# Kernel tuning notes

Hardware: AMD Instinct MI355X
Metric: run time of the kernel (lower is better)

## Reference

```python
import jax, jax.numpy as jnp
import numpy as np
from math import factorial

MAX_L = 2
B = 2
N = 256
TAU = 16


def _cg(j1, j2, j3, m1, m2, m3):
    # standard Clebsch-Gordan coefficient <j1 m1 j2 m2 | j3 m3> (Racah formula)
    if m1 + m2 != m3:
        return 0.0
    f = factorial
    pre = ((2 * j3 + 1) * f(j3 + j1 - j2) * f(j3 - j1 + j2) * f(j1 + j2 - j3) / f(j1 + j2 + j3 + 1)) ** 0.5
    pre *= (f(j3 + m3) * f(j3 - m3) * f(j1 - m1) * f(j1 + m1) * f(j2 - m2) * f(j2 + m2)) ** 0.5
    kmin = max(0, j2 - j3 - m1, j1 - j3 + m2)
    kmax = min(j1 + j2 - j3, j1 - m1, j2 + m2)
    s = 0.0
    for k in range(kmin, kmax + 1):
        s += (-1) ** k / (f(k) * f(j1 + j2 - j3 - k) * f(j1 - m1 - k) * f(j2 + m2 - k) * f(j3 - j2 + m1 + k) * f(j3 - j1 - m2 + k))
    return pre * s


def _cg_table(max_l):
    tab = {}
    for l1 in range(max_l + 1):
        for l2 in range(max_l + 1):
            for l in range(abs(l1 - l2), min(l1 + l2, max_l) + 1):
                C = np.zeros((2 * l1 + 1, 2 * l2 + 1, 2 * l + 1), dtype=np.float32)
                for m1 in range(-l1, l1 + 1):
                    for m2 in range(-l2, l2 + 1):
                        m = m1 + m2
                        if -l <= m <= l:
                            C[m1 + l1, m2 + l2, m + l] = _cg(l1, l2, l, m1, m2, m)
                tab[(l1, l2, l)] = jnp.asarray(C)
    return tab

CG_TAB = _cg_table(MAX_L)


def _cg_product(xs, ys, max_l):
    # xs[l]: [..., 2l+1, t1], ys[l]: [..., 2l+1, t2] -> out[l]: [..., 2l+1, sum t1*t2]
    outs = []
    for l in range(max_l + 1):
        blocks = []
        for l1 in range(max_l + 1):
            for l2 in range(max_l + 1):
                if abs(l1 - l2) <= l <= l1 + l2:
                    C = CG_TAB[(l1, l2, l)]
                    blk = jnp.einsum('...ic,...jd,ijk->...kcd', xs[l1], ys[l2], C)
                    blocks.append(blk.reshape(blk.shape[:-2] + (blk.shape[-2] * blk.shape[-1],)))
        outs.append(jnp.concatenate(blocks, axis=-1))
    return outs


TAU_CG_NL = [3 * TAU * TAU, 6 * TAU * TAU, 6 * TAU * TAU]  # (l1,l2) pair counts: 3,6,6
TAU_CG_REL = [3 * TAU, 6 * TAU, 6 * TAU]


def setup_inputs() -> dict:
    key = jax.random.key(0)
    ks = jax.random.split(key, 14)
    inp = {}
    for l in range(MAX_L + 1):
        inp['v%d' % l] = jax.random.normal(ks[l], (B, N, 1, 2 * l + 1, TAU), dtype=jnp.float32)
        inp['s%d' % l] = jax.random.normal(ks[3 + l], (B, N, N, 2 * l + 1, 1), dtype=jnp.float32)
        inp['wnl%d' % l] = jax.random.normal(ks[6 + l], (TAU_CG_NL[l], TAU), dtype=jnp.float32) * 0.05
        inp['wrel%d' % l] = jax.random.normal(ks[9 + l], (TAU_CG_REL[l], TAU), dtype=jnp.float32) * 0.05
    inp['conn'] = jax.random.randint(ks[13], (B, N, N), 0, 2, dtype=jnp.int32)
    return inp


def reference(v0, v1, v2, conn, s0, s1, s2, wnl0, wnl1, wnl2, wrel0, wrel1, wrel2):
    verts = [v0, v1, v2]
    sph = [s0, s1, s2]
    wnl = [wnl0, wnl1, wnl2]
    wrel = [wrel0, wrel1, wrel2]
    connf = conn.astype(v0.dtype)
    # masked message passing: aggregate neighbor features per node
    vmp = [jnp.einsum('bij,bjxmc->bixmc', connf, v) for v in verts]
    # node-level CG product with itself, then channel mixing
    cg_nl = _cg_product(vmp, vmp, MAX_L)
    mixed_nl = [p @ w for p, w in zip(cg_nl, wnl)]  # [B,N,1,2l+1,TAU]
    # repeat along second array dim to match sph adims [N,N]
    rep = [jnp.broadcast_to(p, (p.shape[0], p.shape[1], N) + p.shape[3:]) for p in mixed_nl]
    # edge-level CG product with spherical harmonics, then channel mixing
    cg_rel = _cg_product(rep, sph, MAX_L)
    mixed_rel = [p @ w for p, w in zip(cg_rel, wrel)]  # [B,N,N,2l+1,TAU]
    # sum over neighbor dim (axis 2), keepdim -> adims back to [N,1]
    summed = [jnp.sum(p, axis=2, keepdims=True) for p in mixed_rel]
    # NormalizeVecArr divides each part in-place by its total sum
    normed = [p / jnp.sum(p) for p in summed]
    return tuple(normed)
```

## Files before the change

kernel.cpp:

```cpp
#include <hip/hip_runtime.h>


#define TAU 16

#define PART_OFF 768
#define VMP_OFF  4096
#define S_OFF    77824
#define WT_OFF   86016

constexpr double cfact(int n){ double r=1.0; for(int i=2;i<=n;i++) r*=i; return r; }
constexpr double csqrt(double x){
  if (x<=0.0) return 0.0;
  double g = x<1.0 ? 1.0 : x;
  for (int i=0;i<80;i++) g = 0.5*(g + x/g);
  return g;
}
constexpr double cg_c(int j1,int j2,int j3,int m1,int m2,int m3){
  if (m1+m2 != m3) return 0.0;
  double pre = csqrt((2.0*j3+1.0)*cfact(j3+j1-j2)*cfact(j3-j1+j2)*cfact(j1+j2-j3)/cfact(j1+j2+j3+1));
  pre *= csqrt(cfact(j3+m3)*cfact(j3-m3)*cfact(j1-m1)*cfact(j1+m1)*cfact(j2-m2)*cfact(j2+m2));
  int kmin = 0;
  if (j2-j3-m1 > kmin) kmin = j2-j3-m1;
  if (j1-j3+m2 > kmin) kmin = j1-j3+m2;
  int kmax = j1+j2-j3;
  if (j1-m1 < kmax) kmax = j1-m1;
  if (j2+m2 < kmax) kmax = j2+m2;
  double s = 0.0;
  for (int k=kmin;k<=kmax;k++){
    double d = cfact(k)*cfact(j1+j2-j3-k)*cfact(j1-m1-k)*cfact(j2+m2-k)*cfact(j3-j2+m1+k)*cfact(j3-j1-m2+k);
    s += (k & 1) ? (-1.0/d) : (1.0/d);
  }
  return pre*s;
}
struct CGTab { float v[615]; };
constexpr CGTab gen_cg(){
  CGTab t{};
  const int TRI[15][3] = {
    {0,0,0},{0,1,1},{0,2,2},{1,0,1},{1,1,0},{1,1,1},{1,1,2},{1,2,1},{1,2,2},
    {2,0,2},{2,1,1},{2,1,2},{2,2,0},{2,2,1},{2,2,2}};
  int off = 0;
  for (int tr=0;tr<15;tr++){
    const int l1=TRI[tr][0], l2=TRI[tr][1], l=TRI[tr][2];
    for (int i1=0;i1<2*l1+1;i1++)
      for (int i2=0;i2<2*l2+1;i2++)
        for (int ik=0;ik<2*l+1;ik++)
          t.v[off++] = (float)cg_c(l1,l2,l,i1-l1,i2-l2,ik-l);
  }
  return t;
}
constexpr CGTab CG = gen_cg();

constexpr int OFF3[27] = {
  0,-1,-1,  -1,1,-1,   -1,-1,10,
  -1,35,-1, 44,53,80,  -1,125,170,
  -1,-1,245,-1,270,315,390,415,490};
constexpr int PAIRS[3][6][2] = {
  {{0,0},{1,1},{2,2},{0,0},{0,0},{0,0}},
  {{0,1},{1,0},{1,1},{1,2},{2,1},{2,2}},
  {{0,2},{1,1},{1,2},{2,0},{2,1},{2,2}}};
constexpr int VOFF[3]   = {0,16,64};
constexpr int SOFF[3]   = {0,1,4};
constexpr int OUT_OFF[3]= {0,8192,32768};
constexpr int NPAIR[3]  = {3,6,6};
constexpr int FOFF[9]   = {0,16,32,48,64,80,96,112,128};
constexpr int WROFF[3]  = {0,768,2304};
constexpr int WTL[3]    = {0,12288,36864};
constexpr int ROWB[3]   = {0,3,21};

__device__ constexpr int RIDX(int l, int mi){ return l==0 ? 0 : (l==1 ? 1+mi : 4+mi); }

__global__ __launch_bounds__(512)
void k_prep(const float* __restrict__ v0, const float* __restrict__ v1, const float* __restrict__ v2,
            const float* __restrict__ s0, const float* __restrict__ s1, const float* __restrict__ s2,
            const float* __restrict__ wnl0, const float* __restrict__ wnl1, const float* __restrict__ wnl2,
            const int* __restrict__ conn, float* __restrict__ ws)
{
  __shared__ float sh_conn[256];
  __shared__ float sh_v[2][144];
  const int t  = threadIdx.x;
  const int bi = blockIdx.x;
  const int b  = bi >> 8;

  if (t < 256) sh_conn[t] = (float)conn[((size_t)bi<<8) + t];
  __syncthreads();

  if (t < 288) {
    const int h = (t >= 144) ? 1 : 0;
    const int tt = t - h*144;
    int l, m, c;
    if (tt < 16)      { l=0; m=0;          c=tt;    }
    else if (tt < 64) { l=1; m=(tt-16)>>4; c=tt&15; }
    else              { l=2; m=(tt-64)>>4; c=tt&15; }
    const float* vl = (l==0) ? v0 : (l==1) ? v1 : v2;
    const int dm = 2*l+1;
    const int stride = dm*TAU;
    const float* base = vl + (((size_t)b*256 + h*128)*dm + m)*TAU + c;
    const float* cr = &sh_conn[h*128];
    float a[8];
    #pragma unroll
    for (int q=0;q<8;q++) a[q]=0.f;
    for (int j=0;j<128;j+=8){
      #pragma unroll
      for (int q=0;q<8;q++) a[q] += cr[j+q]*base[(j+q)*stride];
    }
    sh_v[h][tt] = ((a[0]+a[1])+(a[2]+a[3])) + ((a[4]+a[5])+(a[6]+a[7]));
  } else if (t >= 320 && t < 384) {
    const int lane = t - 320;
    const float* p0 = s0 + (size_t)bi*256;
    const float* p1 = s1 + (size_t)bi*768;
    const float* p2 = s2 + (size_t)bi*1280;
    float a[9];
    #pragma unroll
    for (int m=0;m<9;m++) a[m]=0.f;
    #pragma unroll
    for (int q=0;q<4;q++){
      const int j = lane + q*64;
      a[0] += p0[j];
      a[1] += p1[3*j+0]; a[2] += p1[3*j+1]; a[3] += p1[3*j+2];
      #pragma unroll
      for (int k=0;k<5;k++) a[4+k] += p2[5*j+k];
    }
    #pragma unroll
    for (int m=0;m<9;m++){
      #pragma unroll
      for (int off=32; off; off>>=1) a[m] += __shfl_xor(a[m], off);
    }
    if (lane == 0) {
      #pragma unroll
      for (int m=0;m<9;m++) ws[S_OFF + (size_t)bi*16 + m] = a[m];
    }
  } else if (t >= 448 && bi < 15) {
    const int tile = bi;
    const float* src = (tile<3) ? (wnl0 + (size_t)tile*4096)
                     : (tile<9) ? (wnl1 + (size_t)(tile-3)*4096)
                                : (wnl2 + (size_t)(tile-9)*4096);
    float* dst = ws + WT_OFF + (size_t)tile*4096;
    const int q = t - 448;
    #pragma unroll
    for (int r=0;r<4;r++){
      const int cd = q + r*64;
      const float4 r0 = *(const float4*)(src + cd*16);
      const float4 r1 = *(const float4*)(src + cd*16 + 4);
      const float4 r2 = *(const float4*)(src + cd*16 + 8);
      const float4 r3 = *(const float4*)(src + cd*16 + 12);
      dst[ 0*256+cd]=r0.x; dst[ 1*256+cd]=r0.y; dst[ 2*256+cd]=r0.z; dst[ 3*256+cd]=r0.w;
      dst[ 4*256+cd]=r1.x; dst[ 5*256+cd]=r1.y; dst[ 6*256+cd]=r1.z; dst[ 7*256+cd]=r1.w;
      dst[ 8*256+cd]=r2.x; dst[ 9*256+cd]=r2.y; dst[10*256+cd]=r2.z; dst[11*256+cd]=r2.w;
      dst[12*256+cd]=r3.x; dst[13*256+cd]=r3.y; dst[14*256+cd]=r3.z; dst[15*256+cd]=r3.w;
    }
  }
  __syncthreads();
  if (t < 144) ws[VMP_OFF + (size_t)bi*144 + t] = sh_v[0][t] + sh_v[1][t];
}

template<int L, int P>
__device__ __forceinline__ void build_p(float* __restrict__ dst,
                                        const float (&v_c)[9], const float (&v_d)[9], int tt){
  constexpr int l1 = PAIRS[L][P][0], l2 = PAIRS[L][P][1];
  constexpr int d2 = 2*l2+1, dkk = 2*L+1;
  constexpr int coff = OFF3[l1*9+l2*3+L];
  constexpr int row0 = ROWB[L] + P*dkk;
  #pragma unroll
  for (int kk=0; kk<dkk; kk++){
    const int m = kk - L;
    float a = 0.f;
    #pragma unroll
    for (int m1=-l1; m1<=l1; m1++){
      const int m2 = m - m1;
      if (m2 >= -l2 && m2 <= l2){
        const float C = CG.v[coff + ((m1+l1)*d2 + (m2+l2))*dkk + kk];
        a += C * v_c[RIDX(l1,m1+l1)] * v_d[RIDX(l2,m2+l2)];
      }
    }
    dst[(row0 + kk)*256 + tt] = a;
  }
}

template<int L>
__device__ __forceinline__ void mixl(const float* __restrict__ wt, const float* __restrict__ sh_bm,
                                     float* __restrict__ sh_mnl, int ksub, int tc0){
  constexpr int NP = NPAIR[L];
  constexpr int DK = 2*L+1;
  float acc[DK][2];
  #pragma unroll
  for (int k=0;k<DK;k++){ acc[k][0]=0.f; acc[k][1]=0.f; }
  const float* wb = wt + (size_t)tc0*256 + ksub*4;
  #pragma unroll
  for (int p=0;p<NP;p++){
    const float4 w0 = *(const float4*)(wb + (size_t)p*4096);
    const float4 w1 = *(const float4*)(wb + (size_t)p*4096 + 256);
    #pragma unroll
    for (int k=0;k<DK;k++){
      const float4 bk = *(const float4*)&sh_bm[(ROWB[L] + p*DK + k)*256 + ksub*4];
      acc[k][0] += bk.x*w0.x + bk.y*w0.y + bk.z*w0.z + bk.w*w0.w;
      acc[k][1] += bk.x*w1.x + bk.y*w1.y + bk.z*w1.z + bk.w*w1.w;
    }
  }
  #pragma unroll
  for (int k=0;k<DK;k++){
    #pragma unroll
    for (int off=32; off; off>>=1){
      acc[k][0] += __shfl_xor(acc[k][0], off);
      acc[k][1] += __shfl_xor(acc[k][1], off);
    }
  }
  if (ksub == 0) {
    #pragma unroll
    for (int k=0;k<DK;k++){
      sh_mnl[VOFF[L] + k*16 + tc0    ] = acc[k][0];
      sh_mnl[VOFF[L] + k*16 + tc0 + 1] = acc[k][1];
    }
  }
}

__global__ __launch_bounds__(512, 2)
void k_main(const float* __restrict__ wrel0, const float* __restrict__ wrel1, const float* __restrict__ wrel2,
            const float* __restrict__ ws, float* __restrict__ out, float* __restrict__ part)
{
  __shared__ __align__(16) float sh_bm[51*256];
  __shared__ float sh_wrel[3840];
  __shared__ float sh_mnl[144];
  __shared__ float sh_S[9];
  __shared__ float sh_rel[6*144];
  __shared__ float sh_acc[144];
  __shared__ float sh_lred[48];

  const int t  = threadIdx.x;
  const int bi = blockIdx.x;

  for (int i=t; i<3840; i+=512){
    float v;
    if (i < 768)       v = wrel0[i];
    else if (i < 2304) v = wrel1[i-768];
    else               v = wrel2[i-2304];
    sh_wrel[i] = v;
  }
  const int bc = (t>>4)&15, bd = t&15;
  float v_c[9], v_d[9];
  {
    const float* vb = ws + VMP_OFF + (size_t)bi*144;
    #pragma unroll
    for (int r=0;r<9;r++){ v_c[r] = vb[FOFF[r]+bc]; v_d[r] = vb[FOFF[r]+bd]; }
  }
  if (t < 9) sh_S[t] = ws[S_OFF + (size_t)bi*16 + t];

  const int tg = t>>6, ksub = t&63;
  const int tc0 = tg*2;

  {
    const int tt = t & 255;
    if (t < 256){
      build_p<0,0>(sh_bm,v_c,v_d,tt); build_p<0,1>(sh_bm,v_c,v_d,tt); build_p<0,2>(sh_bm,v_c,v_d,tt);
      build_p<1,0>(sh_bm,v_c,v_d,tt); build_p<1,1>(sh_bm,v_c,v_d,tt); build_p<1,2>(sh_bm,v_c,v_d,tt);
      build_p<2,0>(sh_bm,v_c,v_d,tt); build_p<2,1>(sh_bm,v_c,v_d,tt); build_p<2,2>(sh_bm,v_c,v_d,tt);
    } else {
      build_p<1,3>(sh_bm,v_c,v_d,tt); build_p<1,4>(sh_bm,v_c,v_d,tt); build_p<1,5>(sh_bm,v_c,v_d,tt);
      build_p<2,3>(sh_bm,v_c,v_d,tt); build_p<2,4>(sh_bm,v_c,v_d,tt); build_p<2,5>(sh_bm,v_c,v_d,tt);
    }
  }
  __syncthreads();
  mixl<0>(ws + WT_OFF + WTL[0], sh_bm, sh_mnl, ksub, tc0);
  mixl<1>(ws + WT_OFF + WTL[1], sh_bm, sh_mnl, ksub, tc0);
  mixl<2>(ws + WT_OFF + WTL[2], sh_bm, sh_mnl, ksub, tc0);
  __syncthreads();

  int l=0, f=0;
  if (t < 16)       { l=0; f=t;    }
  else if (t < 64)  { l=1; f=t-16; }
  else if (t < 144) { l=2; f=t-64; }
  const int k = f>>4, tc = f&15;

  if (t < 144) {
    const int np = NPAIR[l];
    #pragma unroll
    for (int p=0; p<6; p++) {
      if (p < np) {
        const int l1 = PAIRS[l][p][0], l2 = PAIRS[l][p][1];
        const int d2 = 2*l2+1;
        const int coff = OFF3[l1*9+l2*3+l];
        const int dk = 2*l+1;
        const int m = k - l;
        float a = 0.f;
        const int lo = (-l1 > m-l2) ? -l1 : m-l2;
        const int hi = ( l1 < m+l2) ?  l1 : m+l2;
        #pragma unroll
        for (int m1=-2; m1<=2; m1++) {
          if (m1 >= lo && m1 <= hi) {
            const int m2 = m - m1;
            const float C = CG.v[coff + ((m1+l1)*d2 + (m2+l2))*dk + k];
            a += C * sh_mnl[VOFF[l1] + (m1+l1)*TAU + tc] * sh_S[SOFF[l2] + (m2+l2)];
          }
        }
        sh_rel[p*144 + t] = a;
      }
    }
  }
  __syncthreads();
  if (t < 144) {
    const int np = NPAIR[l];
    float acc = 0.f;
    #pragma unroll
    for (int p=0; p<6; p++) {
      if (p < np) {
        const float* rrow = &sh_rel[p*144 + VOFF[l] + k*16];
        const float* wrow = &sh_wrel[WROFF[l] + p*256 + tc];
        #pragma unroll
        for (int c=0; c<16; c++)
          acc += rrow[c] * wrow[c*16];
      }
    }
    out[OUT_OFF[l] + ((size_t)bi*(2*l+1) + k)*TAU + tc] = acc;
    sh_acc[t] = acc;
  }
  __syncthreads();
  if (t < 48) {
    const int ll = t>>4, q = t&15;
    const int n = 2*ll+1;
    float a = 0.f;
    for (int i=0;i<n;i++) a += sh_acc[VOFF[ll] + i*16 + q];
    sh_lred[t] = a;
  }
  __syncthreads();
  if (t < 3) {
    float a = 0.f;
    #pragma unroll
    for (int q=0;q<16;q++) a += sh_lred[t*16+q];
    part[t*512 + bi] = a;
  }
}

__global__ __launch_bounds__(256)
void k_norm(float* __restrict__ out, const float* __restrict__ part){
  __shared__ float sh_r[96];
  __shared__ float sh_d[3];
  const int t = threadIdx.x;
  if (t < 96){
    const int l = t>>5, q = t&31;
    const float* p = part + l*512 + q*16;
    float a=0.f;
    #pragma unroll
    for (int i=0;i<16;i++) a += p[i];
    sh_r[t] = a;
  }
  __syncthreads();
  if (t < 3){
    float a=0.f;
    const float* r = &sh_r[t*32];
    #pragma unroll
    for (int i=0;i<32;i++) a += r[i];
    sh_d[t] = a;
  }
  __syncthreads();
  const int idx = blockIdx.x*256 + t;
  if (idx < 73728){
    const int l = (idx < 8192) ? 0 : (idx < 32768) ? 1 : 2;
    out[idx] = out[idx] / sh_d[l];
  }
}

extern "C" void kernel_launch(void* const* d_in, const int* in_sizes, int n_in,
                              void* d_out, int out_size, void* d_ws, size_t ws_size,
                              hipStream_t stream) {
  const float* v0    = (const float*)d_in[0];
  const float* s0    = (const float*)d_in[1];
  const float* wnl0  = (const float*)d_in[2];
  const float* wrel0 = (const float*)d_in[3];
  const float* v1    = (const float*)d_in[4];
  const float* s1    = (const float*)d_in[5];
  const float* wnl1  = (const float*)d_in[6];
  const float* wrel1 = (const float*)d_in[7];
  const float* v2    = (const float*)d_in[8];
  const float* s2    = (const float*)d_in[9];
  const float* wnl2  = (const float*)d_in[10];
  const float* wrel2 = (const float*)d_in[11];
  const int*   conn  = (const int*)d_in[12];
  float* out = (float*)d_out;
  float* ws  = (float*)d_ws;
  float* part = ws + PART_OFF;

  k_prep<<<512, 512, 0, stream>>>(v0, v1, v2, s0, s1, s2,
                                  wnl0, wnl1, wnl2, conn, ws);
  k_main<<<512, 512, 0, stream>>>(wrel0, wrel1, wrel2, ws, out, part);
  k_norm<<<288, 256, 0, stream>>>(out, part);
}
```

Measured before the change: 106.8 us.

## Fuse message-passing prep into main kernel and split weight transpose out

After: 107.7 us. Within noise of the previous version (+0.8%).

```diff
diff --git a/kernel.cpp b/kernel.cpp
--- a/kernel.cpp
+++ b/kernel.cpp
@@ -4,9 +4,7 @@
 #define TAU 16
 
 #define PART_OFF 768
-#define VMP_OFF  4096
-#define S_OFF    77824
-#define WT_OFF   86016
+#define WT_OFF   4096
 
 constexpr double cfact(int n){ double r=1.0; for(int i=2;i<=n;i++) r*=i; return r; }
 constexpr double csqrt(double x){
@@ -69,24 +67,123 @@
 
 __device__ constexpr int RIDX(int l, int mi){ return l==0 ? 0 : (l==1 ? 1+mi : 4+mi); }
 
-__global__ __launch_bounds__(512)
-void k_prep(const float* __restrict__ v0, const float* __restrict__ v1, const float* __restrict__ v2,
+__global__ __launch_bounds__(256)
+void k_wt(const float* __restrict__ wnl0, const float* __restrict__ wnl1, const float* __restrict__ wnl2,
+          float* __restrict__ ws)
+{
+  const int tile = blockIdx.x;
+  const int cd = threadIdx.x;
+  const float* src = (tile<3) ? (wnl0 + (size_t)tile*4096)
+                   : (tile<9) ? (wnl1 + (size_t)(tile-3)*4096)
+                              : (wnl2 + (size_t)(tile-9)*4096);
+  float* dst = ws + WT_OFF + (size_t)tile*4096;
+  const float4 r0 = *(const float4*)(src + cd*16);
+  const float4 r1 = *(const float4*)(src + cd*16 + 4);
+  const float4 r2 = *(const float4*)(src + cd*16 + 8);
+  const float4 r3 = *(const float4*)(src + cd*16 + 12);
+  dst[ 0*256+cd]=r0.x; dst[ 1*256+cd]=r0.y; dst[ 2*256+cd]=r0.z; dst[ 3*256+cd]=r0.w;
+  dst[ 4*256+cd]=r1.x; dst[ 5*256+cd]=r1.y; dst[ 6*256+cd]=r1.z; dst[ 7*256+cd]=r1.w;
+  dst[ 8*256+cd]=r2.x; dst[ 9*256+cd]=r2.y; dst[10*256+cd]=r2.z; dst[11*256+cd]=r2.w;
+  dst[12*256+cd]=r3.x; dst[13*256+cd]=r3.y; dst[14*256+cd]=r3.z; dst[15*256+cd]=r3.w;
+}
+
+template<int L, int P>
+__device__ __forceinline__ void build_p(float* __restrict__ dst,
+                                        const float (&v_c)[9], const float (&v_d)[9], int tt){
+  constexpr int l1 = PAIRS[L][P][0], l2 = PAIRS[L][P][1];
+  constexpr int d2 = 2*l2+1, dkk = 2*L+1;
+  constexpr int coff = OFF3[l1*9+l2*3+L];
+  constexpr int row0 = ROWB[L] + P*dkk;
+  #pragma unroll
+  for (int kk=0; kk<dkk; kk++){
+    const int m = kk - L;
+    float a = 0.f;
+    #pragma unroll
+    for (int m1=-l1; m1<=l1; m1++){
+      const int m2 = m - m1;
+      if (m2 >= -l2 && m2 <= l2){
+        const float C = CG.v[coff + ((m1+l1)*d2 + (m2+l2))*dkk + kk];
+        a += C * v_c[RIDX(l1,m1+l1)] * v_d[RIDX(l2,m2+l2)];
+      }
+    }
+    dst[(row0 + kk)*256 + tt] = a;
+  }
+}
+
+template<int L>
+__device__ __forceinline__ void mixl(const float* __restrict__ wt, const float* __restrict__ sh_bm,
+                                     float* __restrict__ sh_mnl, int ksub, int tc0){
+  constexpr int NP = NPAIR[L];
+  constexpr int DK = 2*L+1;
+  float acc[DK][2];
+  #pragma unroll
+  for (int k=0;k<DK;k++){ acc[k][0]=0.f; acc[k][1]=0.f; }
+  const float* wb = wt + (size_t)tc0*256 + ksub*4;
+  #pragma unroll
+  for (int p=0;p<NP;p++){
+    const float4 w0 = *(const float4*)(wb + (size_t)p*4096);
+    const float4 w1 = *(const float4*)(wb + (size_t)p*4096 + 256);
+    #pragma unroll
+    for (int k=0;k<DK;k++){
+      const float4 bk = *(const float4*)&sh_bm[(ROWB[L] + p*DK + k)*256 + ksub*4];
+      acc[k][0] += bk.x*w0.x + bk.y*w0.y + bk.z*w0.z + bk.w*w0.w;
+      acc[k][1] += bk.x*w1.x + bk.y*w1.y + bk.z*w1.z + bk.w*w1.w;
+    }
+  }
+  #pragma unroll
+  for (int k=0;k<DK;k++){
+    #pragma unroll
+    for (int off=32; off; off>>=1){
+      acc[k][0] += __shfl_xor(acc[k][0], off);
+      acc[k][1] += __shfl_xor(acc[k][1], off);
+    }
+  }
+  if (ksub == 0) {
+    #pragma unroll
+    for (int k=0;k<DK;k++){
+      sh_mnl[VOFF[L] + k*16 + tc0    ] = acc[k][0];
+      sh_mnl[VOFF[L] + k*16 + tc0 + 1] = acc[k][1];
+    }
+  }
+}
+
+__global__ __launch_bounds__(512, 2)
+void k_main(const float* __restrict__ v0, const float* __restrict__ v1, const float* __restrict__ v2,
             const float* __restrict__ s0, const float* __restrict__ s1, const float* __restrict__ s2,
-            const float* __restrict__ wnl0, const float* __restrict__ wnl1, const float* __restrict__ wnl2,
-            const int* __restrict__ conn, float* __restrict__ ws)
+            const float* __restrict__ wrel0, const float* __restrict__ wrel1, const float* __restrict__ wrel2,
+            const int* __restrict__ conn, const float* __restrict__ ws_c,
+            float* __restrict__ out, float* __restrict__ part)
 {
+  __shared__ __align__(16) float sh_bm[51*256];
+  __shared__ float sh_wrel[3840];
   __shared__ float sh_conn[256];
-  __shared__ float sh_v[2][144];
+  __shared__ float sh_v[3][144];
+  __shared__ float sh_vmp[144];
+  __shared__ float sh_mnl[144];
+  __shared__ float sh_S[9];
+  __shared__ float sh_rel[6*144];
+  __shared__ float sh_acc[144];
+  __shared__ float sh_r[48];
+
   const int t  = threadIdx.x;
   const int bi = blockIdx.x;
   const int b  = bi >> 8;
 
   if (t < 256) sh_conn[t] = (float)conn[((size_t)bi<<8) + t];
-  __syncthreads();
-
-  if (t < 288) {
-    const int h = (t >= 144) ? 1 : 0;
+  for (int i=t; i<3840; i+=512){
+    float v;
+    if (i < 768)       v = wrel0[i];
+    else if (i < 2304) v = wrel1[i-768];
+    else               v = wrel2[i-2304];
+    sh_wrel[i] = v;
+  }
+  __syncthreads();
+
+  if (t < 432) {
+    const int h  = (t >= 288) ? 2 : ((t >= 144) ? 1 : 0);
     const int tt = t - h*144;
+    const int j0 = h*86;
+    const int cnt = (h==2) ? 84 : 86;
     int l, m, c;
     if (tt < 16)      { l=0; m=0;          c=tt;    }
     else if (tt < 64) { l=1; m=(tt-16)>>4; c=tt&15; }
@@ -94,18 +191,20 @@
     const float* vl = (l==0) ? v0 : (l==1) ? v1 : v2;
     const int dm = 2*l+1;
     const int stride = dm*TAU;
-    const float* base = vl + (((size_t)b*256 + h*128)*dm + m)*TAU + c;
-    const float* cr = &sh_conn[h*128];
+    const float* base = vl + (((size_t)b*256 + j0)*dm + m)*TAU + c;
+    const float* cr = &sh_conn[j0];
     float a[8];
     #pragma unroll
     for (int q=0;q<8;q++) a[q]=0.f;
-    for (int j=0;j<128;j+=8){
+    int j=0;
+    for (; j+8<=cnt; j+=8){
       #pragma unroll
       for (int q=0;q<8;q++) a[q] += cr[j+q]*base[(j+q)*stride];
     }
+    for (int q=0; j+q<cnt; q++) a[q] += cr[j+q]*base[(j+q)*stride];
     sh_v[h][tt] = ((a[0]+a[1])+(a[2]+a[3])) + ((a[4]+a[5])+(a[6]+a[7]));
-  } else if (t >= 320 && t < 384) {
-    const int lane = t - 320;
+  } else if (t >= 448) {
+    const int lane = t - 448;
     const float* p0 = s0 + (size_t)bi*256;
     const float* p1 = s1 + (size_t)bi*768;
     const float* p2 = s2 + (size_t)bi*1280;
@@ -127,122 +226,17 @@
     }
     if (lane == 0) {
       #pragma unroll
-      for (int m=0;m<9;m++) ws[S_OFF + (size_t)bi*16 + m] = a[m];
-    }
-  } else if (t >= 448 && bi < 15) {
-    const int tile = bi;
-    const float* src = (tile<3) ? (wnl0 + (size_t)tile*4096)
-                     : (tile<9) ? (wnl1 + (size_t)(tile-3)*4096)
-                                : (wnl2 + (size_t)(tile-9)*4096);
-    float* dst = ws + WT_OFF + (size_t)tile*4096;
-    const int q = t - 448;
-    #pragma unroll
-    for (int r=0;r<4;r++){
-      const int cd = q + r*64;
-      const float4 r0 = *(const float4*)(src + cd*16);
-      const float4 r1 = *(const float4*)(src + cd*16 + 4);
-      const float4 r2 = *(const float4*)(src + cd*16 + 8);
-      const float4 r3 = *(const float4*)(src + cd*16 + 12);
-      dst[ 0*256+cd]=r0.x; dst[ 1*256+cd]=r0.y; dst[ 2*256+cd]=r0.z; dst[ 3*256+cd]=r0.w;
-      dst[ 4*256+cd]=r1.x; dst[ 5*256+cd]=r1.y; dst[ 6*256+cd]=r1.z; dst[ 7*256+cd]=r1.w;
-      dst[ 8*256+cd]=r2.x; dst[ 9*256+cd]=r2.y; dst[10*256+cd]=r2.z; dst[11*256+cd]=r2.w;
-      dst[12*256+cd]=r3.x; dst[13*256+cd]=r3.y; dst[14*256+cd]=r3.z; dst[15*256+cd]=r3.w;
-    }
-  }
-  __syncthreads();
-  if (t < 144) ws[VMP_OFF + (size_t)bi*144 + t] = sh_v[0][t] + sh_v[1][t];
-}
-
-template<int L, int P>
-__device__ __forceinline__ void build_p(float* __restrict__ dst,
-                                        const float (&v_c)[9], const float (&v_d)[9], int tt){
-  constexpr int l1 = PAIRS[L][P][0], l2 = PAIRS[L][P][1];
-  constexpr int d2 = 2*l2+1, dkk = 2*L+1;
-  constexpr int coff = OFF3[l1*9+l2*3+L];
-  constexpr int row0 = ROWB[L] + P*dkk;
-  #pragma unroll
-  for (int kk=0; kk<dkk; kk++){
-    const int m = kk - L;
-    float a = 0.f;
-    #pragma unroll
-    for (int m1=-l1; m1<=l1; m1++){
-      const int m2 = m - m1;
-      if (m2 >= -l2 && m2 <= l2){
-        const float C = CG.v[coff + ((m1+l1)*d2 + (m2+l2))*dkk + kk];
-        a += C * v_c[RIDX(l1,m1+l1)] * v_d[RIDX(l2,m2+l2)];
-      }
-    }
-    dst[(row0 + kk)*256 + tt] = a;
-  }
-}
-
-template<int L>
-__device__ __forceinline__ void mixl(const float* __restrict__ wt, const float* __restrict__ sh_bm,
-                                     float* __restrict__ sh_mnl, int ksub, int tc0){
-  constexpr int NP = NPAIR[L];
-  constexpr int DK = 2*L+1;
-  float acc[DK][2];
-  #pragma unroll
-  for (int k=0;k<DK;k++){ acc[k][0]=0.f; acc[k][1]=0.f; }
-  const float* wb = wt + (size_t)tc0*256 + ksub*4;
-  #pragma unroll
-  for (int p=0;p<NP;p++){
-    const float4 w0 = *(const float4*)(wb + (size_t)p*4096);
-    const float4 w1 = *(const float4*)(wb + (size_t)p*4096 + 256);
-    #pragma unroll
-    for (int k=0;k<DK;k++){
-      const float4 bk = *(const float4*)&sh_bm[(ROWB[L] + p*DK + k)*256 + ksub*4];
-      acc[k][0] += bk.x*w0.x + bk.y*w0.y + bk.z*w0.z + bk.w*w0.w;
-      acc[k][1] += bk.x*w1.x + bk.y*w1.y + bk.z*w1.z + bk.w*w1.w;
-    }
-  }
-  #pragma unroll
-  for (int k=0;k<DK;k++){
-    #pragma unroll
-    for (int off=32; off; off>>=1){
-      acc[k][0] += __shfl_xor(acc[k][0], off);
-      acc[k][1] += __shfl_xor(acc[k][1], off);
-    }
-  }
-  if (ksub == 0) {
-    #pragma unroll
-    for (int k=0;k<DK;k++){
-      sh_mnl[VOFF[L] + k*16 + tc0    ] = acc[k][0];
-      sh_mnl[VOFF[L] + k*16 + tc0 + 1] = acc[k][1];
-    }
-  }
-}
-
-__global__ __launch_bounds__(512, 2)
-void k_main(const float* __restrict__ wrel0, const float* __restrict__ wrel1, const float* __restrict__ wrel2,
-            const float* __restrict__ ws, float* __restrict__ out, float* __restrict__ part)
-{
-  __shared__ __align__(16) float sh_bm[51*256];
-  __shared__ float sh_wrel[3840];
-  __shared__ float sh_mnl[144];
-  __shared__ float sh_S[9];
-  __shared__ float sh_rel[6*144];
-  __shared__ float sh_acc[144];
-  __shared__ float sh_lred[48];
-
-  const int t  = threadIdx.x;
-  const int bi = blockIdx.x;
-
-  for (int i=t; i<3840; i+=512){
-    float v;
-    if (i < 768)       v = wrel0[i];
-    else if (i < 2304) v = wrel1[i-768];
-    else               v = wrel2[i-2304];
-    sh_wrel[i] = v;
-  }
+      for (int m=0;m<9;m++) sh_S[m] = a[m];
+    }
+  }
+  __syncthreads();
+  if (t < 144) sh_vmp[t] = (sh_v[0][t] + sh_v[1][t]) + sh_v[2][t];
+  __syncthreads();
+
   const int bc = (t>>4)&15, bd = t&15;
   float v_c[9], v_d[9];
-  {
-    const float* vb = ws + VMP_OFF + (size_t)bi*144;
-    #pragma unroll
-    for (int r=0;r<9;r++){ v_c[r] = vb[FOFF[r]+bc]; v_d[r] = vb[FOFF[r]+bd]; }
-  }
-  if (t < 9) sh_S[t] = ws[S_OFF + (size_t)bi*16 + t];
+  #pragma unroll
+  for (int r=0;r<9;r++){ v_c[r] = sh_vmp[FOFF[r]+bc]; v_d[r] = sh_vmp[FOFF[r]+bd]; }
 
   const int tg = t>>6, ksub = t&63;
   const int tc0 = tg*2;
@@ -259,9 +253,9 @@
     }
   }
   __syncthreads();
-  mixl<0>(ws + WT_OFF + WTL[0], sh_bm, sh_mnl, ksub, tc0);
-  mixl<1>(ws + WT_OFF + WTL[1], sh_bm, sh_mnl, ksub, tc0);
-  mixl<2>(ws + WT_OFF + WTL[2], sh_bm, sh_mnl, ksub, tc0);
+  mixl<0>(ws_c + WT_OFF + WTL[0], sh_bm, sh_mnl, ksub, tc0);
+  mixl<1>(ws_c + WT_OFF + WTL[1], sh_bm, sh_mnl, ksub, tc0);
+  mixl<2>(ws_c + WT_OFF + WTL[2], sh_bm, sh_mnl, ksub, tc0);
   __syncthreads();
 
   int l=0, f=0;
@@ -318,13 +312,13 @@
     const int n = 2*ll+1;
     float a = 0.f;
     for (int i=0;i<n;i++) a += sh_acc[VOFF[ll] + i*16 + q];
-    sh_lred[t] = a;
+    sh_r[t] = a;
   }
   __syncthreads();
   if (t < 3) {
     float a = 0.f;
     #pragma unroll
-    for (int q=0;q<16;q++) a += sh_lred[t*16+q];
+    for (int q=0;q<16;q++) a += sh_r[t*16+q];
     part[t*512 + bi] = a;
   }
 }
@@ -351,10 +345,12 @@
     sh_d[t] = a;
   }
   __syncthreads();
-  const int idx = blockIdx.x*256 + t;
-  if (idx < 73728){
-    const int l = (idx < 8192) ? 0 : (idx < 32768) ? 1 : 2;
-    out[idx] = out[idx] / sh_d[l];
+  const int i4 = blockIdx.x*256 + t;
+  if (i4 < 18432){
+    const float dd = (i4 < 2048) ? sh_d[0] : ((i4 < 8192) ? sh_d[1] : sh_d[2]);
+    float4 v = ((const float4*)out)[i4];
+    v.x/=dd; v.y/=dd; v.z/=dd; v.w/=dd;
+    ((float4*)out)[i4] = v;
   }
 }
 
@@ -378,8 +374,8 @@
   float* ws  = (float*)d_ws;
   float* part = ws + PART_OFF;
 
-  k_prep<<<512, 512, 0, stream>>>(v0, v1, v2, s0, s1, s2,
-                                  wnl0, wnl1, wnl2, conn, ws);
-  k_main<<<512, 512, 0, stream>>>(wrel0, wrel1, wrel2, ws, out, part);
-  k_norm<<<288, 256, 0, stream>>>(out, part);
-}
+  k_wt  <<<15,  256, 0, stream>>>(wnl0, wnl1, wnl2, ws);
+  k_main<<<512, 512, 0, stream>>>(v0, v1, v2, s0, s1, s2,
+                                  wrel0, wrel1, wrel2, conn, ws, out, part);
+  k_norm<<<72,  256, 0, stream>>>(out, part);
+}
```
